# Optimization experiments

Measured on AMD Instinct MI355X. Metric: run time of the kernel, lower is better.

The kernel has to match this reference:

```python
import jax, jax.numpy as jnp
import numpy as np

B, V, H, L = 2, 256, 128, 3
GROUPS = 32  # GroupNorm32 in the 'normalization' head
EPS = 1e-5


def _layernorm(z, g, b):
    m = jnp.mean(z, -1, keepdims=True)
    v = jnp.var(z, -1, keepdims=True)
    return (z - m) * jax.lax.rsqrt(v + EPS) * g + b


def _forward(x, adj_matrix, emb_type, W_node, b_node, W_eattr, b_eattr, W_ee, b_ee,
             Wu, bu, Wv, bv, Wa, ba, Wb, bb, Wc, bc,
             lnh_g, lnh_b, lne_g, lne_b, plo_g, plo_b, plo_W, plo_bW,
             gn_g, gn_b, W_out, b_out):
    # node embed: Embedding(2,H) lookup -> Linear(H,H)
    h = emb_type[x] @ W_node + b_node                      # B V H
    ea = jnp.transpose(adj_matrix, (0, 2, 3, 1))           # B V V 6
    # edge embed: Linear(6,H) -> Linear(H,H)
    e = (ea @ W_eattr + b_eattr) @ W_ee + b_ee             # B V V H
    # graph = graph[..., -6].long(): binary adjacency channel, no grad
    mask = jax.lax.stop_gradient(ea[..., 0])               # B V V
    for l in range(L):
        h_in, e_in = h, e
        # gated anisotropic GCN layer (DIFUSCO GNNLayer, mode='direct')
        Uh = h @ Wu[l] + bu[l]                             # B V H
        Vh = h @ Wv[l] + bv[l]                             # B V H
        e_new = ((h @ Wa[l] + ba[l])[:, None, :, :]
                 + (h @ Wb[l] + bb[l])[:, :, None, :]
                 + (e @ Wc[l] + bc[l]))                    # B V V H
        gates = jax.nn.sigmoid(e_new) * mask[..., None]    # B V V H
        agg = jnp.einsum('bijh,bjh->bih', gates, Vh)       # gated 'sum' aggregation
        h = jax.nn.relu(_layernorm(Uh + agg, lnh_g[l], lnh_b[l]))
        e = jax.nn.relu(_layernorm(e_new, lne_g[l], lne_b[l]))
        # outer residual (GNNDi.dense_forward) + per_layer_out: LN -> SiLU -> Linear
        h = h_in + h
        e = e_in + (jax.nn.silu(_layernorm(e, plo_g[l], plo_b[l])) @ plo_W[l] + plo_bW[l])
    # head: GroupNorm(32,H) -> ReLU -> Conv2d(H, out_channels, 1) on B H V V
    z = jnp.transpose(e, (0, 3, 1, 2))                     # B H V V
    zg = z.reshape(B, GROUPS, H // GROUPS, V, V)
    mu = jnp.mean(zg, axis=(2, 3, 4), keepdims=True)
    var = jnp.var(zg, axis=(2, 3, 4), keepdims=True)
    z = ((zg - mu) * jax.lax.rsqrt(var + EPS)).reshape(B, H, V, V)
    z = jax.nn.relu(z * gn_g[None, :, None, None] + gn_b[None, :, None, None])
    return jnp.einsum('bchw,oc->bohw', z, W_out) + b_out[None, :, None, None]


def setup_inputs() -> dict:
    key = jax.random.key(0)
    ks = jax.random.split(key, 16)
    nrm = lambda k, s: jax.random.normal(k, s, dtype=jnp.float32) * 0.05
    adj = jnp.concatenate([
        (jax.random.uniform(ks[1], (B, 1, V, V)) < 0.15).astype(jnp.float32),  # channel 0: adjacency
        jax.random.normal(ks[2], (B, 5, V, V), dtype=jnp.float32)], axis=1)
    return {
        'x': jax.random.randint(ks[0], (B, V), 0, 2),
        'adj_matrix': adj,
        'emb_type': nrm(ks[3], (2, H)),
        'W_node': nrm(ks[4], (H, H)), 'b_node': jnp.zeros((H,), jnp.float32),
        'W_eattr': nrm(ks[5], (6, H)), 'b_eattr': jnp.zeros((H,), jnp.float32),
        'W_ee': nrm(ks[6], (H, H)), 'b_ee': jnp.zeros((H,), jnp.float32),
        'Wu': nrm(ks[7], (L, H, H)), 'bu': jnp.zeros((L, H), jnp.float32),
        'Wv': nrm(ks[8], (L, H, H)), 'bv': jnp.zeros((L, H), jnp.float32),
        'Wa': nrm(ks[9], (L, H, H)), 'ba': jnp.zeros((L, H), jnp.float32),
        'Wb': nrm(ks[10], (L, H, H)), 'bb': jnp.zeros((L, H), jnp.float32),
        'Wc': nrm(ks[11], (L, H, H)), 'bc': jnp.zeros((L, H), jnp.float32),
        'lnh_g': jnp.ones((L, H), jnp.float32), 'lnh_b': jnp.zeros((L, H), jnp.float32),
        'lne_g': jnp.ones((L, H), jnp.float32), 'lne_b': jnp.zeros((L, H), jnp.float32),
        'plo_g': jnp.ones((L, H), jnp.float32), 'plo_b': jnp.zeros((L, H), jnp.float32),
        'plo_W': nrm(ks[12], (L, H, H)), 'plo_bW': jnp.zeros((L, H), jnp.float32),
        'gn_g': jnp.ones((H,), jnp.float32), 'gn_b': jnp.zeros((H,), jnp.float32),
        'W_out': nrm(ks[13], (1, H)), 'b_out': jnp.zeros((1,), jnp.float32),
    }


def reference(x, adj_matrix, emb_type, W_node, b_node, W_eattr, b_eattr, W_ee, b_ee,
              Wu, bu, Wv, bv, Wa, ba, Wb, bb, Wc, bc,
              lnh_g, lnh_b, lne_g, lne_b, plo_g, plo_b, plo_W, plo_bW,
              gn_g, gn_b, W_out, b_out):
    return _forward(x, adj_matrix, emb_type, W_node, b_node, W_eattr, b_eattr, W_ee, b_ee,
                    Wu, bu, Wv, bv, Wa, ba, Wb, bb, Wc, bc,
                    lnh_g, lnh_b, lne_g, lne_b, plo_g, plo_b, plo_W, plo_bW,
                    gn_g, gn_b, W_out, b_out)
```

## Files before the change

### kernel.cpp

```cpp
#include <hip/hip_runtime.h>
#include <cstdint>
#include <cstddef>


#define EPSV 1e-5f

typedef __attribute__((ext_vector_type(8))) short short8v;
typedef __attribute__((ext_vector_type(4))) float f32x4;

__device__ __forceinline__ float sigmoidf_(float x) { return 1.f / (1.f + __expf(-x)); }

__device__ __forceinline__ unsigned short f2bf(float x) {
    unsigned int u = __float_as_uint(x);
    unsigned int r = u + 0x7FFFu + ((u >> 16) & 1u);
    return (unsigned short)(r >> 16);
}
__device__ __forceinline__ float bf2f(unsigned short u) {
    return __uint_as_float(((unsigned int)u) << 16);
}
__device__ __forceinline__ unsigned int cvtpk(float a, float b) {
    unsigned int r;
    asm("v_cvt_pk_bf16_f32 %0, %1, %2" : "=v"(r) : "v"(a), "v"(b));
    return r;
}
#define SWZ(row, cb) ((cb) ^ (((row) & 7) << 4))

__global__ void k_prep(const int* __restrict__ x, const float* __restrict__ emb,
                       const float* __restrict__ W_node, const float* __restrict__ b_node,
                       float* __restrict__ h, float* __restrict__ aggB,
                       const float* __restrict__ W_ea, const float* __restrict__ b_ea,
                       const float* __restrict__ W_ee, const float* __restrict__ b_ee,
                       float* __restrict__ Wcb, float* __restrict__ bcb,
                       const float* __restrict__ Wc, const float* __restrict__ PW,
                       unsigned short* __restrict__ WT)
{
    const int blk = blockIdx.x, t = threadIdx.x;
    if (blk < 512) {
        __shared__ float se[128];
        if (t < 128) { se[t] = emb[x[blk]*128 + t]; aggB[blk*128 + t] = 0.f; }
        __syncthreads();
        if (t < 128) {
            float acc = b_node[t];
            for (int k = 0; k < 128; ++k) acc = fmaf(se[k], W_node[k*128+t], acc);
            h[blk*128+t] = acc;
        }
    } else if (blk == 512) {
        if (t < 128) {
            float wc0=0,wc1=0,wc2=0,wc3=0,wc4=0,wc5=0,bv=0;
            for (int m = 0; m < 128; ++m) {
                float we = W_ee[m*128 + t];
                wc0 = fmaf(W_ea[0*128+m], we, wc0);
                wc1 = fmaf(W_ea[1*128+m], we, wc1);
                wc2 = fmaf(W_ea[2*128+m], we, wc2);
                wc3 = fmaf(W_ea[3*128+m], we, wc3);
                wc4 = fmaf(W_ea[4*128+m], we, wc4);
                wc5 = fmaf(W_ea[5*128+m], we, wc5);
                bv  = fmaf(b_ea[m], we, bv);
            }
            Wcb[0*128+t]=wc0; Wcb[1*128+t]=wc1; Wcb[2*128+t]=wc2;
            Wcb[3*128+t]=wc3; Wcb[4*128+t]=wc4; Wcb[5*128+t]=wc5;
            bcb[t] = bv + b_ee[t];
        }
    } else {
        const int m = blk - 513;
        const int l = m >> 1;
        const float* src = (m & 1) ? (PW + (size_t)l*16384) : (Wc + (size_t)l*16384);
        unsigned short* dst = WT + (size_t)m*16384;
        for (int idx = t; idx < 16384; idx += 256) {
            int n = idx >> 7, k = idx & 127;
            dst[idx] = f2bf(src[k*128 + n]);
        }
    }
}

__global__ void k_hgemm(float* __restrict__ h, float* __restrict__ Uh, float* __restrict__ aggB,
    const float* __restrict__ Wu_l, const float* __restrict__ bu_l,
    const float* __restrict__ Wv_l, const float* __restrict__ bv_l,
    const float* __restrict__ Wa_l, const float* __restrict__ ba_l,
    const float* __restrict__ Wb_l, const float* __restrict__ bb_l,
    float* __restrict__ Vh, float* __restrict__ Ah, float* __restrict__ Bh,
    const float* __restrict__ lnh_g, const float* __restrict__ lnh_b, int upd)
{
    __shared__ float sh[128];
    __shared__ float sred[4];
    int blk = blockIdx.x, t = threadIdx.x;
    float hv_ = h[blk*128 + t];
    if (upd) {
        float val = Uh[blk*128 + t] + aggB[blk*128 + t];
        aggB[blk*128 + t] = 0.f;
        float s = val, q = val*val;
        #pragma unroll
        for (int off = 32; off; off >>= 1) { s += __shfl_down(s, off); q += __shfl_down(q, off); }
        if ((t & 63) == 0) { sred[t>>6] = s; sred[2 + (t>>6)] = q; }
        __syncthreads();
        s = sred[0] + sred[1]; q = sred[2] + sred[3];
        float mean = s * (1.f/128.f);
        float var  = q * (1.f/128.f) - mean*mean;
        float nv = (val - mean) * rsqrtf(var + EPSV) * lnh_g[t] + lnh_b[t];
        hv_ += fmaxf(nv, 0.f);
        h[blk*128 + t] = hv_;
    }
    sh[t] = hv_;
    __syncthreads();
    float au=bu_l[t], av=bv_l[t], aa=ba_l[t], ab=bb_l[t];
    for (int k = 0; k < 128; ++k) {
        float hv = sh[k];
        au = fmaf(hv, Wu_l[k*128+t], au);
        av = fmaf(hv, Wv_l[k*128+t], av);
        aa = fmaf(hv, Wa_l[k*128+t], aa);
        ab = fmaf(hv, Wb_l[k*128+t], ab);
    }
    Uh[blk*128+t]=au; Bh[blk*128+t]=ab;
    Vh[blk*128+t]=av; Ah[blk*128+t]=aa;
}

template<int EINIT, int DO_AGG, int DO_STATS>
__global__ __launch_bounds__(256) void k_layer(
    unsigned short* __restrict__ e,
    const unsigned short* __restrict__ WcT, const unsigned short* __restrict__ PWT,
    const float* __restrict__ bc_l,
    const float* __restrict__ Ah, const float* __restrict__ Bh,
    const float* __restrict__ Vh, const float* __restrict__ adj,
    const float* __restrict__ lne_g, const float* __restrict__ lne_b,
    const float* __restrict__ plo_g, const float* __restrict__ plo_b,
    const float* __restrict__ pbW_l,
    float* __restrict__ aggB,
    const float* __restrict__ Wcb, const float* __restrict__ bcb,
    float* __restrict__ ggsum, float* __restrict__ ggsq)
{
    __shared__ __align__(16) char sW[32768];
    __shared__ float sRedA[512];
    __shared__ float sRedB[128];

    const int t = threadIdx.x;
    const int bi = blockIdx.x >> 2, chunk = blockIdx.x & 3;
    const int b = bi >> 8, i = bi & 255;
    const int w = t >> 6, lane = t & 63;
    const int lane16 = lane & 15, g = lane >> 4;
    const size_t rowbase = (size_t)bi * 32768;
    const int j0 = chunk*64 + w*16;
    char* sE = sW + w*4096;

    short8v a8[4];
    if (EINIT) {
        float am[6];
        const float* adjp = adj + (size_t)b*393216 + (size_t)i*256 + (j0 + lane16);
        #pragma unroll
        for (int m = 0; m < 6; ++m) am[m] = adjp[(size_t)m*65536];
        unsigned short* erow = &e[rowbase + (size_t)(j0 + lane16)*128];
        #pragma unroll
        for (int kst = 0; kst < 4; ++kst) {
            const int base = kst*32 + g*8;
            float4 v0 = *(const float4*)&bcb[base];
            float4 v1 = *(const float4*)&bcb[base+4];
            float vv[8] = {v0.x, v0.y, v0.z, v0.w, v1.x, v1.y, v1.z, v1.w};
            #pragma unroll
            for (int m = 0; m < 6; ++m) {
                const float4 w0 = *(const float4*)&Wcb[m*128 + base];
                const float4 w1 = *(const float4*)&Wcb[m*128 + base + 4];
                vv[0] = fmaf(am[m], w0.x, vv[0]); vv[1] = fmaf(am[m], w0.y, vv[1]);
                vv[2] = fmaf(am[m], w0.z, vv[2]); vv[3] = fmaf(am[m], w0.w, vv[3]);
                vv[4] = fmaf(am[m], w1.x, vv[4]); vv[5] = fmaf(am[m], w1.y, vv[5]);
                vv[6] = fmaf(am[m], w1.z, vv[6]); vv[7] = fmaf(am[m], w1.w, vv[7]);
            }
            short8v vfr;
            #pragma unroll
            for (int pr = 0; pr < 4; ++pr) {
                const unsigned int p = cvtpk(vv[pr*2], vv[pr*2+1]);
                vfr[pr*2]   = (short)(unsigned short)p;
                vfr[pr*2+1] = (short)(unsigned short)(p >> 16);
            }
            a8[kst] = vfr;
            *(short8v*)&erow[base] = vfr;
        }
    } else {
        const unsigned short* arow = e + rowbase + (size_t)(j0 + lane16)*128 + g*8;
        #pragma unroll
        for (int kst = 0; kst < 4; ++kst)
            a8[kst] = *(const short8v*)&arow[kst*32];
    }

    #pragma unroll
    for (int p = 0; p < 8; ++p) {
        const int idx = t*8 + p*2048;
        const int n = idx >> 7, cb = (idx & 127) << 1;
        *(short8v*)(sW + n*256 + SWZ(n, cb)) = *(const short8v*)&WcT[idx];
    }
    __syncthreads();

    f32x4 tv[8];
    float agg[8];
    float s1[4] = {0,0,0,0}, q1[4] = {0,0,0,0};
    const int jb = j0 + g*4;
    float4 mk;
    if (DO_AGG) mk = *(const float4*)&adj[(size_t)b*393216 + (size_t)i*256 + jb];
    const float* mkp = (const float*)&mk;
    #pragma unroll
    for (int nt = 0; nt < 8; ++nt) {
        const int col = nt*16 + lane16;
        f32x4 acc = {0.f,0.f,0.f,0.f};
        #pragma unroll
        for (int kst = 0; kst < 4; ++kst) {
            short8v bfr = *(const short8v*)(sW + col*256 + SWZ(col, kst*64 + g*16));
            acc = __builtin_amdgcn_mfma_f32_16x16x32_bf16(a8[kst], bfr, acc, 0, 0, 0);
        }
        const float bcB = bc_l[col] + Bh[bi*128 + col];
        if (DO_AGG) {
            float a = 0.f;
            #pragma unroll
            for (int r = 0; r < 4; ++r) {
                const float ahv = Ah[(size_t)(b*256 + jb + r)*128 + col];
                const float vhv = Vh[(size_t)(b*256 + jb + r)*128 + col];
                float tvl = acc[r] + bcB + ahv;
                a = fmaf(mkp[r]*sigmoidf_(tvl), vhv, a);
                s1[r] += tvl; q1[r] = fmaf(tvl, tvl, q1[r]);
                tv[nt][r] = tvl;
            }
            agg[nt] = a;
        } else {
            #pragma unroll
            for (int r = 0; r < 4; ++r) {
                const float ahv = Ah[(size_t)(b*256 + jb + r)*128 + col];
                float tvl = acc[r] + bcB + ahv;
                s1[r] += tvl; q1[r] = fmaf(tvl, tvl, q1[r]);
                tv[nt][r] = tvl;
            }
        }
    }
    float mu1[4], rs1[4];
    #pragma unroll
    for (int r = 0; r < 4; ++r) {
        float s = s1[r], q = q1[r];
        s += __shfl_xor(s,1); q += __shfl_xor(q,1);
        s += __shfl_xor(s,2); q += __shfl_xor(q,2);
        s += __shfl_xor(s,4); q += __shfl_xor(q,4);
        s += __shfl_xor(s,8); q += __shfl_xor(q,8);
        float mu = s*(1.f/128.f);
        mu1[r] = mu; rs1[r] = rsqrtf(q*(1.f/128.f) - mu*mu + EPSV);
    }
    float s2[4] = {0,0,0,0}, q2[4] = {0,0,0,0};
    #pragma unroll
    for (int nt = 0; nt < 8; ++nt) {
        const int col = nt*16 + lane16;
        const float lg = lne_g[col], lb = lne_b[col];
        #pragma unroll
        for (int r = 0; r < 4; ++r) {
            float tp = fmaxf(fmaf((tv[nt][r]-mu1[r])*rs1[r], lg, lb), 0.f);
            tv[nt][r] = tp;
            s2[r] += tp; q2[r] = fmaf(tp, tp, q2[r]);
        }
    }
    float mu2[4], rs2[4];
    #pragma unroll
    for (int r = 0; r < 4; ++r) {
        float s = s2[r], q = q2[r];
        s += __shfl_xor(s,1); q += __shfl_xor(q,1);
        s += __shfl_xor(s,2); q += __shfl_xor(q,2);
        s += __shfl_xor(s,4); q += __shfl_xor(q,4);
        s += __shfl_xor(s,8); q += __shfl_xor(q,8);
        float mu = s*(1.f/128.f);
        mu2[r] = mu; rs2[r] = rsqrtf(q*(1.f/128.f) - mu*mu + EPSV);
    }

    __syncthreads();

    #pragma unroll
    for (int nt = 0; nt < 8; ++nt) {
        const int col = nt*16 + lane16;
        const float pg = plo_g[col], pb = plo_b[col];
        float u[4];
        #pragma unroll
        for (int r = 0; r < 4; ++r) {
            float uu = fmaf((tv[nt][r]-mu2[r])*rs2[r], pg, pb);
            u[r] = uu * sigmoidf_(uu);
        }
        const unsigned int p01 = cvtpk(u[0], u[1]);
        const unsigned int p23 = cvtpk(u[2], u[3]);
        const int r0 = g*4;
        *(unsigned short*)(sE + (r0+0)*256 + SWZ(r0+0, col*2)) = (unsigned short)p01;
        *(unsigned short*)(sE + (r0+1)*256 + SWZ(r0+1, col*2)) = (unsigned short)(p01 >> 16);
        *(unsigned short*)(sE + (r0+2)*256 + SWZ(r0+2, col*2)) = (unsigned short)p23;
        *(unsigned short*)(sE + (r0+3)*256 + SWZ(r0+3, col*2)) = (unsigned short)(p23 >> 16);
    }
    short8v b8[4];
    #pragma unroll
    for (int kst = 0; kst < 4; ++kst)
        b8[kst] = *(const short8v*)(sE + lane16*256 + SWZ(lane16, kst*64 + g*16));

    __syncthreads();
    #pragma unroll
    for (int p = 0; p < 8; ++p) {
        const int idx = t*8 + p*2048;
        const int n = idx >> 7, cb = (idx & 127) << 1;
        *(short8v*)(sW + n*256 + SWZ(n, cb)) = *(const short8v*)&PWT[idx];
    }
    __syncthreads();

    const int jg = j0 + lane16;
    float gs[8], gq[8];
    #pragma unroll
    for (int nt = 0; nt < 8; ++nt) {
        const int an = nt*16 + lane16;
        f32x4 acc = {0.f,0.f,0.f,0.f};
        #pragma unroll
        for (int kst = 0; kst < 4; ++kst) {
            short8v aw = *(const short8v*)(sW + an*256 + SWZ(an, kst*64 + g*16));
            acc = __builtin_amdgcn_mfma_f32_16x16x32_bf16(aw, b8[kst], acc, 0, 0, 0);
        }
        const int n0 = nt*16 + g*4;
        const float4 pw4 = *(const float4*)&pbW_l[n0];
        const float* pwp = (const float*)&pw4;
        unsigned short* ep = &e[rowbase + (size_t)jg*128 + n0];
        const ushort4 ev = *(const ushort4*)ep;
        const float o0 = acc[0] + (pwp[0] + bf2f(ev.x));
        const float o1 = acc[1] + (pwp[1] + bf2f(ev.y));
        const float o2 = acc[2] + (pwp[2] + bf2f(ev.z));
        const float o3 = acc[3] + (pwp[3] + bf2f(ev.w));
        if (DO_STATS) {
            gs[nt] = (o0 + o1) + (o2 + o3);
            gq[nt] = fmaf(o0,o0, fmaf(o1,o1, fmaf(o2,o2, o3*o3)));
        }
        uint2 st;
        st.x = cvtpk(o0, o1);
        st.y = cvtpk(o2, o3);
        *(uint2*)ep = st;
    }

    if (DO_AGG) {
        #pragma unroll
        for (int nt = 0; nt < 8; ++nt) {
            float a = agg[nt];
            a += __shfl_xor(a, 16); a += __shfl_xor(a, 32);
            if (lane < 16) sRedA[w*128 + nt*16 + lane] = a;
        }
        __syncthreads();
        if (t < 128) {
            float S = sRedA[t] + sRedA[128+t] + sRedA[256+t] + sRedA[384+t];
            atomicAdd(&aggB[bi*128 + t], S);
        }
    }
    if (DO_STATS) {
        #pragma unroll
        for (int nt = 0; nt < 8; ++nt) {
            float a = gs[nt], qq = gq[nt];
            a += __shfl_xor(a, 1); qq += __shfl_xor(qq, 1);
            a += __shfl_xor(a, 2); qq += __shfl_xor(qq, 2);
            a += __shfl_xor(a, 4); qq += __shfl_xor(qq, 4);
            a += __shfl_xor(a, 8); qq += __shfl_xor(qq, 8);
            if (lane16 == 0) {
                sRedA[w*32 + nt*4 + g] = a;
                sRedB[w*32 + nt*4 + g] = qq;
            }
        }
        __syncthreads();
        if (t < 32) {
            float S = sRedA[t] + sRedA[32+t] + sRedA[64+t] + sRedA[96+t];
            float Q = sRedB[t] + sRedB[32+t] + sRedB[64+t] + sRedB[96+t];
            atomicAdd(&ggsum[b*32 + t], S);
            atomicAdd(&ggsq[b*32 + t], Q);
        }
    }
}

__global__ void k_gfin(const float* __restrict__ ggsum, const float* __restrict__ ggsq,
                       float* __restrict__ gmu, float* __restrict__ grs)
{
    int t = threadIdx.x;
    float s = ggsum[t], q = ggsq[t];
    const float invN = 1.f/(4.f*65536.f);
    float mu = s*invN;
    float var = q*invN - mu*mu;
    gmu[t] = mu;
    grs[t] = rsqrtf(var + EPSV);
}

__global__ __launch_bounds__(256) void k_head(
    const unsigned short* __restrict__ e, const float* __restrict__ gmu,
    const float* __restrict__ grs, const float* __restrict__ gn_g,
    const float* __restrict__ gn_b, const float* __restrict__ W_out,
    const float* __restrict__ b_out, float* __restrict__ out)
{
    const int blk = blockIdx.x, t = threadIdx.x;
    const int b = blk >> 8;
    const int ch8 = (t & 15)*8, jgrp = t >> 4;
    float gg[8], gb[8], wo[8];
    #pragma unroll
    for (int c = 0; c < 8; ++c) {
        const int ch = ch8 + c;
        const float mu = gmu[b*32 + (ch>>2)], rs = grs[b*32 + (ch>>2)];
        gg[c] = gn_g[ch]*rs;
        gb[c] = gn_b[ch] - mu*gg[c];
        wo[c] = W_out[ch];
    }
    const float bo = b_out[0];
    const unsigned short* erow = e + (size_t)blk*32768;
    float* orow = out + (size_t)blk*256;
    for (int it = 0; it < 16; ++it) {
        const int j = jgrp*16 + it;
        short8v v = *(const short8v*)&erow[(size_t)j*128 + ch8];
        float p = 0.f;
        #pragma unroll
        for (int c = 0; c < 8; ++c) {
            float f = bf2f((unsigned short)v[c]);
            p = fmaf(fmaxf(fmaf(f, gg[c], gb[c]), 0.f), wo[c], p);
        }
        p += __shfl_xor(p, 1); p += __shfl_xor(p, 2);
        p += __shfl_xor(p, 4); p += __shfl_xor(p, 8);
        if ((t & 15) == 0) orow[j] = p + bo;
    }
}

extern "C" void kernel_launch(void* const* d_in, const int* in_sizes, int n_in,
                              void* d_out, int out_size, void* d_ws, size_t ws_size,
                              hipStream_t stream)
{
    const int*   x      = (const int*)  d_in[0];
    const float* adj    = (const float*)d_in[1];
    const float* emb    = (const float*)d_in[2];
    const float* W_node = (const float*)d_in[3];
    const float* b_node = (const float*)d_in[4];
    const float* W_ea   = (const float*)d_in[5];
    const float* b_ea   = (const float*)d_in[6];
    const float* W_ee   = (const float*)d_in[7];
    const float* b_ee   = (const float*)d_in[8];
    const float* Wu     = (const float*)d_in[9];
    const float* bu     = (const float*)d_in[10];
    const float* Wv     = (const float*)d_in[11];
    const float* bv     = (const float*)d_in[12];
    const float* Wa     = (const float*)d_in[13];
    const float* ba     = (const float*)d_in[14];
    const float* Wb     = (const float*)d_in[15];
    const float* bb     = (const float*)d_in[16];
    const float* Wc     = (const float*)d_in[17];
    const float* bc     = (const float*)d_in[18];
    const float* lnh_g  = (const float*)d_in[19];
    const float* lnh_b  = (const float*)d_in[20];
    const float* lne_g  = (const float*)d_in[21];
    const float* lne_b  = (const float*)d_in[22];
    const float* plo_g  = (const float*)d_in[23];
    const float* plo_b  = (const float*)d_in[24];
    const float* plo_W  = (const float*)d_in[25];
    const float* plo_bW = (const float*)d_in[26];
    const float* gn_g   = (const float*)d_in[27];
    const float* gn_b   = (const float*)d_in[28];
    const float* W_out  = (const float*)d_in[29];
    const float* b_out  = (const float*)d_in[30];
    float* out = (float*)d_out;

    float* ws = (float*)d_ws;
    size_t off = 0;
    unsigned short* e = (unsigned short*)(ws + off); off += 8388608;
    float* h    = ws + off; off += 65536;
    float* Uh   = ws + off; off += 65536;
    float* Bh   = ws + off; off += 65536;
    float* Vh   = ws + off; off += 65536;
    float* Ah   = ws + off; off += 65536;
    float* aggB = ws + off; off += 65536;
    float* Wcb  = ws + off; off += 768;
    float* bcb  = ws + off; off += 128;
    float* ggsum = ws + off; off += 64;
    float* ggsq  = ws + off; off += 64;
    float* gmu  = ws + off; off += 64;
    float* grs  = ws + off; off += 64;
    unsigned short* WT = (unsigned short*)(ws + off); off += 49152;

    k_prep<<<519, 256, 0, stream>>>(x, emb, W_node, b_node, h, aggB,
                                    W_ea, b_ea, W_ee, b_ee, Wcb, bcb,
                                    Wc, plo_W, WT);
    hipMemsetAsync(ggsum, 0, 512, stream);

    for (int l = 0; l < 3; ++l) {
        k_hgemm<<<512, 128, 0, stream>>>(h, Uh, aggB,
            Wu + (size_t)l*16384, bu + l*128,
            Wv + (size_t)l*16384, bv + l*128,
            Wa + (size_t)l*16384, ba + l*128,
            Wb + (size_t)l*16384, bb + l*128,
            Vh, Ah, Bh,
            lnh_g + (l==0?0:(l-1)*128), lnh_b + (l==0?0:(l-1)*128), l > 0 ? 1 : 0);
        const unsigned short* WcT_l = WT + (size_t)(2*l)*16384;
        const unsigned short* PWT_l = WT + (size_t)(2*l+1)*16384;
        if (l == 0) {
            k_layer<1,1,0><<<2048, 256, 0, stream>>>(e, WcT_l, PWT_l,
                bc + l*128, Ah, Bh, Vh, adj,
                lne_g + l*128, lne_b + l*128,
                plo_g + l*128, plo_b + l*128,
                plo_bW + l*128, aggB, Wcb, bcb, ggsum, ggsq);
        } else if (l == 1) {
            k_layer<0,1,0><<<2048, 256, 0, stream>>>(e, WcT_l, PWT_l,
                bc + l*128, Ah, Bh, Vh, adj,
                lne_g + l*128, lne_b + l*128,
                plo_g + l*128, plo_b + l*128,
                plo_bW + l*128, aggB, Wcb, bcb, ggsum, ggsq);
        } else {
            k_layer<0,0,1><<<2048, 256, 0, stream>>>(e, WcT_l, PWT_l,
                bc + l*128, Ah, Bh, Vh, adj,
                lne_g + l*128, lne_b + l*128,
                plo_g + l*128, plo_b + l*128,
                plo_bW + l*128, aggB, Wcb, bcb, ggsum, ggsq);
        }
    }

    k_gfin<<<1, 64, 0, stream>>>(ggsum, ggsq, gmu, grs);
    k_head<<<512, 256, 0, stream>>>(e, gmu, grs, gn_g, gn_b, W_out, b_out, out);
}
```

Before: 212.5 us.

## Pre-pack weights in MFMA fragment order and read them directly from global

The prep kernel now writes the transposed Wc and per-layer-out weights in the exact per-lane MFMA fragment order. The layer kernel reads B/A fragments straight from global/L2 with coalesced 16-byte loads instead of staging 32KB into LDS with barriers. This shrinks LDS use from 32KB to 16KB per block, which may raise occupancy, and removes several __syncthreads. In exchange every wave re-reads the weights from cache rather than sharing them through LDS.

```diff
diff --git a/kernel.cpp b/kernel.cpp
--- a/kernel.cpp
+++ b/kernel.cpp
@@ -67,7 +67,13 @@
         const float* src = (m & 1) ? (PW + (size_t)l*16384) : (Wc + (size_t)l*16384);
         unsigned short* dst = WT + (size_t)m*16384;
         for (int idx = t; idx < 16384; idx += 256) {
-            int n = idx >> 7, k = idx & 127;
+            const int frag  = idx >> 9;
+            const int lane  = (idx >> 3) & 63;
+            const int e2    = idx & 7;
+            const int nt = frag >> 2, kst = frag & 3;
+            const int lane16 = lane & 15, g = lane >> 4;
+            const int n = nt*16 + lane16;
+            const int k = kst*32 + g*8 + e2;
             dst[idx] = f2bf(src[k*128 + n]);
         }
     }
@@ -117,7 +123,7 @@
 template<int EINIT, int DO_AGG, int DO_STATS>
 __global__ __launch_bounds__(256) void k_layer(
     unsigned short* __restrict__ e,
-    const unsigned short* __restrict__ WcT, const unsigned short* __restrict__ PWT,
+    const unsigned short* __restrict__ WcF, const unsigned short* __restrict__ PWF,
     const float* __restrict__ bc_l,
     const float* __restrict__ Ah, const float* __restrict__ Bh,
     const float* __restrict__ Vh, const float* __restrict__ adj,
@@ -128,7 +134,7 @@
     const float* __restrict__ Wcb, const float* __restrict__ bcb,
     float* __restrict__ ggsum, float* __restrict__ ggsq)
 {
-    __shared__ __align__(16) char sW[32768];
+    __shared__ __align__(16) char sUa[16384];
     __shared__ float sRedA[512];
     __shared__ float sRedB[128];
 
@@ -139,7 +145,7 @@
     const int lane16 = lane & 15, g = lane >> 4;
     const size_t rowbase = (size_t)bi * 32768;
     const int j0 = chunk*64 + w*16;
-    char* sE = sW + w*4096;
+    char* sE = sUa + w*4096;
 
     short8v a8[4];
     if (EINIT) {
@@ -173,20 +179,13 @@
             a8[kst] = vfr;
             *(short8v*)&erow[base] = vfr;
         }
+        __syncthreads();
     } else {
         const unsigned short* arow = e + rowbase + (size_t)(j0 + lane16)*128 + g*8;
         #pragma unroll
         for (int kst = 0; kst < 4; ++kst)
             a8[kst] = *(const short8v*)&arow[kst*32];
     }
-
-    #pragma unroll
-    for (int p = 0; p < 8; ++p) {
-        const int idx = t*8 + p*2048;
-        const int n = idx >> 7, cb = (idx & 127) << 1;
-        *(short8v*)(sW + n*256 + SWZ(n, cb)) = *(const short8v*)&WcT[idx];
-    }
-    __syncthreads();
 
     f32x4 tv[8];
     float agg[8];
@@ -201,7 +200,7 @@
         f32x4 acc = {0.f,0.f,0.f,0.f};
         #pragma unroll
         for (int kst = 0; kst < 4; ++kst) {
-            short8v bfr = *(const short8v*)(sW + col*256 + SWZ(col, kst*64 + g*16));
+            short8v bfr = *(const short8v*)&WcF[((nt*4+kst) << 9) + (lane << 3)];
             acc = __builtin_amdgcn_mfma_f32_16x16x32_bf16(a8[kst], bfr, acc, 0, 0, 0);
         }
         const float bcB = bc_l[col] + Bh[bi*128 + col];
@@ -262,8 +261,6 @@
         mu2[r] = mu; rs2[r] = rsqrtf(q*(1.f/128.f) - mu*mu + EPSV);
     }
 
-    __syncthreads();
-
     #pragma unroll
     for (int nt = 0; nt < 8; ++nt) {
         const int col = nt*16 + lane16;
@@ -287,24 +284,14 @@
     for (int kst = 0; kst < 4; ++kst)
         b8[kst] = *(const short8v*)(sE + lane16*256 + SWZ(lane16, kst*64 + g*16));
 
-    __syncthreads();
-    #pragma unroll
-    for (int p = 0; p < 8; ++p) {
-        const int idx = t*8 + p*2048;
-        const int n = idx >> 7, cb = (idx & 127) << 1;
-        *(short8v*)(sW + n*256 + SWZ(n, cb)) = *(const short8v*)&PWT[idx];
-    }
-    __syncthreads();
-
     const int jg = j0 + lane16;
     float gs[8], gq[8];
     #pragma unroll
     for (int nt = 0; nt < 8; ++nt) {
-        const int an = nt*16 + lane16;
         f32x4 acc = {0.f,0.f,0.f,0.f};
         #pragma unroll
         for (int kst = 0; kst < 4; ++kst) {
-            short8v aw = *(const short8v*)(sW + an*256 + SWZ(an, kst*64 + g*16));
+            short8v aw = *(const short8v*)&PWF[((nt*4+kst) << 9) + (lane << 3)];
             acc = __builtin_amdgcn_mfma_f32_16x16x32_bf16(aw, b8[kst], acc, 0, 0, 0);
         }
         const int n0 = nt*16 + g*4;
@@ -477,22 +464,22 @@
             Wb + (size_t)l*16384, bb + l*128,
             Vh, Ah, Bh,
             lnh_g + (l==0?0:(l-1)*128), lnh_b + (l==0?0:(l-1)*128), l > 0 ? 1 : 0);
-        const unsigned short* WcT_l = WT + (size_t)(2*l)*16384;
-        const unsigned short* PWT_l = WT + (size_t)(2*l+1)*16384;
+        const unsigned short* WcF_l = WT + (size_t)(2*l)*16384;
+        const unsigned short* PWF_l = WT + (size_t)(2*l+1)*16384;
         if (l == 0) {
-            k_layer<1,1,0><<<2048, 256, 0, stream>>>(e, WcT_l, PWT_l,
+            k_layer<1,1,0><<<2048, 256, 0, stream>>>(e, WcF_l, PWF_l,
                 bc + l*128, Ah, Bh, Vh, adj,
                 lne_g + l*128, lne_b + l*128,
                 plo_g + l*128, plo_b + l*128,
                 plo_bW + l*128, aggB, Wcb, bcb, ggsum, ggsq);
         } else if (l == 1) {
-            k_layer<0,1,0><<<2048, 256, 0, stream>>>(e, WcT_l, PWT_l,
+            k_layer<0,1,0><<<2048, 256, 0, stream>>>(e, WcF_l, PWF_l,
                 bc + l*128, Ah, Bh, Vh, adj,
                 lne_g + l*128, lne_b + l*128,
                 plo_g + l*128, plo_b + l*128,
                 plo_bW + l*128, aggB, Wcb, bcb, ggsum, ggsq);
         } else {
-            k_layer<0,0,1><<<2048, 256, 0, stream>>>(e, WcT_l, PWT_l,
+            k_layer<0,0,1><<<2048, 256, 0, stream>>>(e, WcF_l, PWF_l,
                 bc + l*128, Ah, Bh, Vh, adj,
                 lne_g + l*128, lne_b + l*128,
                 plo_g + l*128, plo_b + l*128,
```

Result: slower. 255.3 us (+20.1%).
